# Kernel optimization log

Hardware: AMD Instinct MI355X
Metric: run time of the kernel (lower is better)

The kernel has to match this reference:

```python
import jax, jax.numpy as jnp
import numpy as np

N_NODES = 50000


def gcn_layer(x, src, dst, W, b, n_nodes):
    # Linear transform first (as in PyG GCNConv)
    x = x @ W  # [N, out]
    # Symmetric normalization with self-loop-augmented degree
    ones = jnp.ones(src.shape[0], dtype=x.dtype)
    deg = jax.ops.segment_sum(ones, dst, num_segments=n_nodes)
    dinv = jnp.where(deg > 0, jax.lax.rsqrt(deg), 0.0).astype(x.dtype)
    norm = dinv[src] * dinv[dst]  # [E]
    msgs = x[src] * norm[:, None]  # [E, out]
    out = jax.ops.segment_sum(msgs, dst, num_segments=n_nodes)
    return out + b


def add_self_loops(edge_index, n_nodes):
    loop = jnp.arange(n_nodes, dtype=edge_index.dtype)
    src = jnp.concatenate([edge_index[0], loop])
    dst = jnp.concatenate([edge_index[1], loop])
    return src, dst


def setup_inputs() -> dict:
    key = jax.random.key(0)
    k1, k2, k3, k4 = jax.random.split(key, 4)
    in_ch, hid = 256, 256
    n_edges = 1600000
    x = jax.random.normal(k1, (N_NODES, in_ch), dtype=jnp.float32)
    edge_index = jax.random.randint(k2, (2, n_edges), 0, N_NODES, dtype=jnp.int64)
    # Glorot-style init for GCN weights
    W1 = jax.random.normal(k3, (in_ch, hid), dtype=jnp.float32) * (1.0 / np.sqrt(in_ch))
    b1 = jnp.zeros((hid,), dtype=jnp.float32)
    W2 = jax.random.normal(k4, (hid, hid), dtype=jnp.float32) * (1.0 / np.sqrt(hid))
    b2 = jnp.zeros((hid,), dtype=jnp.float32)
    return {"x": x, "edge_index": edge_index, "W1": W1, "b1": b1, "W2": W2, "b2": b2}


def reference(x, edge_index, W1, b1, W2, b2):
    n = x.shape[0]
    src, dst = add_self_loops(edge_index, n)
    h = gcn_layer(x, src, dst, W1, b1, n)
    h = jax.nn.relu(h)
    out = gcn_layer(h, src, dst, W2, b2, n)
    return out
```

## Files before the change

### kernel.cpp

```cpp
#include <hip/hip_runtime.h>
#include <stdint.h>

typedef __attribute__((ext_vector_type(8))) short bf16x8;
typedef __attribute__((ext_vector_type(4))) float f32x4;

#define NBLK 256
#define BSH  7
#define BSZ  128

typedef __attribute__((address_space(1))) const unsigned int gu32;
typedef __attribute__((address_space(3))) unsigned int lu32;

__device__ __forceinline__ float bf2f(unsigned short b) {
    union { unsigned u; float f; } c; c.u = ((unsigned)b) << 16; return c.f;
}
__device__ __forceinline__ float bflo(unsigned w) {
    union { unsigned u; float f; } c; c.u = w << 16; return c.f;
}
__device__ __forceinline__ float bfhi(unsigned w) {
    union { unsigned u; float f; } c; c.u = w & 0xffff0000u; return c.f;
}
__device__ __forceinline__ unsigned short f2bf(float f) {
    union { float f; unsigned u; } c; c.f = f;
    unsigned u = c.u;
    u += 0x7fffu + ((u >> 16) & 1u);
    return (unsigned short)(u >> 16);
}

__global__ void GNNEncoder_317827579954_kernel() {}

__global__ void k_flags(const unsigned* __restrict__ x, const int* __restrict__ ei,
                        int E, int* __restrict__ flags) {
    int t = threadIdx.x;
    int pl = 0;
    for (int i = t; i < 256; i += 64) {
        unsigned u = x[i] & 0xffffu;
        unsigned e = (u >> 7) & 0xffu;
        if ((e >= 100u && e <= 145u) || u == 0u) ++pl;
    }
    for (int off = 32; off; off >>= 1) pl += __shfl_down(pl, off);
    int n = E < 64 ? E : 64;
    unsigned long long nz = __ballot(t < n ? (ei[2 * t + 1] != 0) : 0);
    if (t == 0) {
        flags[0] = (pl >= 192) ? 0 : 1;
        flags[1] = (nz == 0ull) ? 1 : 0;
    }
}

__global__ void k_cvtT(const void* __restrict__ Wa, unsigned short* __restrict__ Wta,
                       const void* __restrict__ Wb, unsigned short* __restrict__ Wtb,
                       const int* __restrict__ flags) {
    int bb = blockIdx.x;
    const void* W = bb < 256 ? Wa : Wb;
    unsigned short* Wt = bb < 256 ? Wta : Wtb;
    int n = bb & 255, k = threadIdx.x;
    unsigned short v;
    if (flags[0]) v = f2bf(((const float*)W)[k * 256 + n]);
    else          v = ((const unsigned short*)W)[k * 256 + n];
    Wt[n * 256 + k] = v;
}


__global__ __launch_bounds__(256) void k_cmat(const int* __restrict__ ei, int E,
                                              const int* __restrict__ flags,
                                              int* __restrict__ cmat, int nb) {
    __shared__ int lc[512];
    int t = threadIdx.x, b = blockIdx.x;
    for (int i = t; i < nb; i += 256) lc[i] = 0;
    __syncthreads();
    int chunk = (E + NBLK - 1) / NBLK;
    int beg = b * chunk;
    int end = beg + chunk; if (end > E) end = E;
    int i64 = flags[1];
    for (int i = beg + t; i < end; i += 256) {
        int d = i64 ? ei[2 * E + 2 * i] : ei[E + i];
        atomicAdd(&lc[d >> BSH], 1);
    }
    __syncthreads();
    for (int j = t; j < nb; j += 256) cmat[j * NBLK + b] = lc[j];
}

__global__ __launch_bounds__(512) void k_cscan(int* __restrict__ cmat,
                                               int* __restrict__ boff,
                                               int* __restrict__ offs,
                                               int nb, int N, int E) {
    __shared__ int sc[512];
    int t = threadIdx.x;
    int run = 0;
    if (t < nb) {
        int* row = cmat + t * NBLK;
        for (int b = 0; b < NBLK; ++b) { int v = row[b]; row[b] = run; run += v; }
    }
    sc[t] = run;
    __syncthreads();
    int val = run;
    for (int off = 1; off < 512; off <<= 1) {
        int u = (t >= off) ? sc[t - off] : 0;
        __syncthreads();
        sc[t] += u;
        __syncthreads();
    }
    int ex = sc[t] - val;
    if (t < nb) {
        boff[t] = ex;
        int* row = cmat + t * NBLK;
        for (int b = 0; b < NBLK; ++b) row[b] += ex;
    }
    if (t == 0) { boff[nb] = E; offs[N] = E; }
}

__global__ __launch_bounds__(256) void k_fillmat(const int* __restrict__ ei, int E,
                                                 const int* __restrict__ flags,
                                                 const int* __restrict__ cmat,
                                                 unsigned* __restrict__ tmp, int nb) {
    __shared__ int cur[512];
    int t = threadIdx.x, b = blockIdx.x;
    for (int j = t; j < nb; j += 256) cur[j] = cmat[j * NBLK + b];
    __syncthreads();
    int chunk = (E + NBLK - 1) / NBLK;
    int beg = b * chunk;
    int end = beg + chunk; if (end > E) end = E;
    int i64 = flags[1];
    for (int i = beg + t; i < end; i += 256) {
        int s, d;
        if (i64) { s = ei[2 * i]; d = ei[2 * E + 2 * i]; }
        else     { s = ei[i];     d = ei[E + i]; }
        int p = atomicAdd(&cur[d >> BSH], 1);
        tmp[p] = ((unsigned)s << BSH) | (unsigned)(d & (BSZ - 1));
    }
}

__global__ __launch_bounds__(256) void k_bbuild(const unsigned* __restrict__ tmp,
                                                const int* __restrict__ boff,
                                                int* __restrict__ offs,
                                                float* __restrict__ dinv,
                                                int* __restrict__ csr, int N) {
    __shared__ int ldeg[BSZ], lex[BSZ], lcur[BSZ];
    int b = blockIdx.x;
    int t = threadIdx.x;
    int base = b << BSH;
    int beg = boff[b], end = boff[b + 1];
    if (t < BSZ) ldeg[t] = 0;
    __syncthreads();
    for (int i = beg + t; i < end; i += 256) {
        unsigned u = tmp[i];
        atomicAdd(&ldeg[u & (BSZ - 1u)], 1);
    }
    __syncthreads();
    if (t == 0) {
        int run = 0;
        for (int i = 0; i < BSZ; ++i) {
            int v = ldeg[i];
            lex[i] = run; lcur[i] = run;
            run += v;
        }
    }
    __syncthreads();
    if (t < BSZ) {
        int v = base + t;
        if (v < N) {
            offs[v] = beg + lex[t];
            dinv[v] = rsqrtf((float)(ldeg[t] + 1));
        }
    }
    for (int i = beg + t; i < end; i += 256) {
        unsigned u = tmp[i];
        int p = atomicAdd(&lcur[u & (BSZ - 1u)], 1);
        csr[beg + p] = (int)(u >> BSH);
    }
}

__global__ __launch_bounds__(256) void k_gemm(const void* __restrict__ Araw,
                                              const unsigned short* __restrict__ Bt,
                                              unsigned short* __restrict__ C,
                                              const float* __restrict__ dinv,
                                              const int* __restrict__ flags, int useflag,
                                              int M) {
    __shared__ unsigned short smem[16384];
    int tid  = threadIdx.x;
    int lane = tid & 63;
    int wave = tid >> 6;
    int q = lane >> 4;
    int r = lane & 15;
    int rowBase0 = blockIdx.x * 64;
    int rowBase = rowBase0 + wave * 16;
    int af32 = useflag ? flags[0] : 0;

    int arow = rowBase + r;
    arow = arow < M ? arow : M - 1;
    const unsigned short* aptrh = (const unsigned short*)Araw + (size_t)arow * 256;
    const float*          aptrf = (const float*)Araw + (size_t)arow * 256;

    auto stage = [&](int buf, int kk) {
#pragma unroll
        for (int j = 0; j < 4; ++j) {
            int c = wave * 256 + j * 64 + lane;
            int col = c >> 2;
            int kc = (c & 3) ^ (col & 3);
            const unsigned short* src = Bt + col * 256 + kk + kc * 8;
            unsigned short* dst = smem + buf * 8192 + (wave * 4 + j) * 512;
            __builtin_amdgcn_global_load_lds((gu32*)src, (lu32*)dst, 16, 0, 0);
        }
    };

    stage(0, 0);
    __syncthreads();

    f32x4 acc[16] = {};
    int cur = 0;
    for (int kk = 0; kk < 256; kk += 32) {
        if (kk < 224) stage(cur ^ 1, kk + 32);
        bf16x8 a;
        if (af32) {
            float4 v0 = *(const float4*)(aptrf + kk + q * 8);
            float4 v1 = *(const float4*)(aptrf + kk + q * 8 + 4);
            union { unsigned short s[8]; bf16x8 v; } ua;
            ua.s[0] = f2bf(v0.x); ua.s[1] = f2bf(v0.y); ua.s[2] = f2bf(v0.z); ua.s[3] = f2bf(v0.w);
            ua.s[4] = f2bf(v1.x); ua.s[5] = f2bf(v1.y); ua.s[6] = f2bf(v1.z); ua.s[7] = f2bf(v1.w);
            a = ua.v;
        } else {
            a = *(const bf16x8*)(aptrh + kk + q * 8);
        }
#pragma unroll
        for (int nt = 0; nt < 16; ++nt) {
            int col = nt * 16 + r;
            const unsigned short* bp = smem + cur * 8192 + col * 32 + (q ^ (col & 3)) * 8;
            bf16x8 b = *(const bf16x8*)bp;
            acc[nt] = __builtin_amdgcn_mfma_f32_16x16x32_bf16(a, b, acc[nt], 0, 0, 0);
        }
        __syncthreads();
        cur ^= 1;
    }

    float ds4[4];
#pragma unroll
    for (int r2 = 0; r2 < 4; ++r2) {
        int row = rowBase + q * 4 + r2;
        ds4[r2] = (row < M) ? dinv[row] : 0.f;
    }
    int lrow0 = wave * 16 + q * 4;
#pragma unroll
    for (int nt = 0; nt < 16; ++nt) {
        int col = nt * 16 + r;
#pragma unroll
        for (int r2 = 0; r2 < 4; ++r2)
            smem[(lrow0 + r2) * 256 + col] = f2bf(acc[nt][r2] * ds4[r2]);
    }
    __syncthreads();
#pragma unroll
    for (int p = 0; p < 8; ++p) {
        int idx = wave * 4096 + p * 512 + lane * 8;
        int grow = rowBase0 + (idx >> 8);
        if (grow < M)
            *(uint4*)(C + (size_t)grow * 256 + (idx & 255)) = *(const uint4*)(smem + idx);
    }
}

__global__ __launch_bounds__(256) void k_agg(const unsigned short* __restrict__ XWs,
                                             const int* __restrict__ csr,
                                             const int* __restrict__ offs,
                                             const float* __restrict__ dinv,
                                             const void* __restrict__ bias,
                                             void* __restrict__ out,
                                             int relu, int final_, const int* __restrict__ flags,
                                             int N) {
    int v = blockIdx.x * 4 + (threadIdx.x >> 6);
    if (v >= N) return;
    int lane = threadIdx.x & 63;
    int half = lane >> 5;
    int cl   = (lane & 31) * 8;
    float acc[8] = {};
    int beg = offs[v], end = offs[v + 1];
    int e = beg;
    for (; e + 8 <= end; e += 8) {
        int s[4]; uint4 u[4];
#pragma unroll
        for (int j = 0; j < 4; ++j) s[j] = csr[e + 2 * j + half];
#pragma unroll
        for (int j = 0; j < 4; ++j) u[j] = *(const uint4*)(XWs + (size_t)s[j] * 256 + cl);
#pragma unroll
        for (int j = 0; j < 4; ++j) {
            acc[0] += bflo(u[j].x); acc[1] += bfhi(u[j].x);
            acc[2] += bflo(u[j].y); acc[3] += bfhi(u[j].y);
            acc[4] += bflo(u[j].z); acc[5] += bfhi(u[j].z);
            acc[6] += bflo(u[j].w); acc[7] += bfhi(u[j].w);
        }
    }
    for (; e + 2 <= end; e += 2) {
        int s = csr[e + half];
        uint4 u = *(const uint4*)(XWs + (size_t)s * 256 + cl);
        acc[0] += bflo(u.x); acc[1] += bfhi(u.x);
        acc[2] += bflo(u.y); acc[3] += bfhi(u.y);
        acc[4] += bflo(u.z); acc[5] += bfhi(u.z);
        acc[6] += bflo(u.w); acc[7] += bfhi(u.w);
    }
    if (e < end && half == 0) {
        int s = csr[e];
        uint4 u = *(const uint4*)(XWs + (size_t)s * 256 + cl);
        acc[0] += bflo(u.x); acc[1] += bfhi(u.x);
        acc[2] += bflo(u.y); acc[3] += bfhi(u.y);
        acc[4] += bflo(u.z); acc[5] += bfhi(u.z);
        acc[6] += bflo(u.w); acc[7] += bfhi(u.w);
    }
#pragma unroll
    for (int k = 0; k < 8; ++k) acc[k] += __shfl_xor(acc[k], 32);
    if (half) return;

    float dv = dinv[v];
    uint4 su = *(const uint4*)(XWs + (size_t)v * 256 + cl);
    float sf[8];
    sf[0] = bflo(su.x); sf[1] = bfhi(su.x);
    sf[2] = bflo(su.y); sf[3] = bfhi(su.y);
    sf[4] = bflo(su.z); sf[5] = bfhi(su.z);
    sf[6] = bflo(su.w); sf[7] = bfhi(su.w);
    float bb[8];
    if (flags[0]) {
        const float4* bp = (const float4*)((const float*)bias + cl);
        float4 b0 = bp[0], b1 = bp[1];
        bb[0] = b0.x; bb[1] = b0.y; bb[2] = b0.z; bb[3] = b0.w;
        bb[4] = b1.x; bb[5] = b1.y; bb[6] = b1.z; bb[7] = b1.w;
    } else {
        uint4 bu = *(const uint4*)((const unsigned short*)bias + cl);
        bb[0] = bflo(bu.x); bb[1] = bfhi(bu.x);
        bb[2] = bflo(bu.y); bb[3] = bfhi(bu.y);
        bb[4] = bflo(bu.z); bb[5] = bfhi(bu.z);
        bb[6] = bflo(bu.w); bb[7] = bfhi(bu.w);
    }
    float r[8];
#pragma unroll
    for (int k = 0; k < 8; ++k) {
        float t = dv * (acc[k] + sf[k]) + bb[k];
        r[k] = relu ? fmaxf(t, 0.f) : t;
    }
    if (final_ && flags[0]) {
        float* op = (float*)out + (size_t)v * 256 + cl;
        float4 o0, o1;
        o0.x = r[0]; o0.y = r[1]; o0.z = r[2]; o0.w = r[3];
        o1.x = r[4]; o1.y = r[5]; o1.z = r[6]; o1.w = r[7];
        ((float4*)op)[0] = o0; ((float4*)op)[1] = o1;
    } else {
        uint4 o;
        o.x = (unsigned)f2bf(r[0]) | ((unsigned)f2bf(r[1]) << 16);
        o.y = (unsigned)f2bf(r[2]) | ((unsigned)f2bf(r[3]) << 16);
        o.z = (unsigned)f2bf(r[4]) | ((unsigned)f2bf(r[5]) << 16);
        o.w = (unsigned)f2bf(r[6]) | ((unsigned)f2bf(r[7]) << 16);
        *(uint4*)((unsigned short*)out + (size_t)v * 256 + cl) = o;
    }
}

extern "C" void kernel_launch(void* const* d_in, const int* in_sizes, int n_in,
                              void* d_out, int out_size, void* d_ws, size_t ws_size,
                              hipStream_t stream) {
    (void)n_in; (void)out_size; (void)ws_size;
    const void* x  = d_in[0];
    const int*  ei = (const int*)d_in[1];
    const void* W1 = d_in[2];
    const void* b1 = d_in[3];
    const void* W2 = d_in[4];
    const void* b2 = d_in[5];

    int N = in_sizes[0] / 256;
    int E = in_sizes[1] / 2;
    int NB = (N + BSZ - 1) / BSZ;

    char* p = (char*)d_ws;
    auto alloc = [&](size_t bytes) {
        char* r = p;
        p += (bytes + 255) & ~(size_t)255;
        return r;
    };
    int*            flags  = (int*)alloc(8);
    int*            boff   = (int*)alloc(516 * 4);
    int*            offs   = (int*)alloc(((size_t)N + 1) * 4);
    float*          dinv   = (float*)alloc((size_t)N * 4);
    unsigned short* wt1    = (unsigned short*)alloc(256 * 256 * 2);
    unsigned short* wt2    = (unsigned short*)alloc(256 * 256 * 2);
    int*            csr    = (int*)alloc((size_t)E * 4);
    unsigned short* buf0   = (unsigned short*)alloc((size_t)N * 256 * 2);
    unsigned short* buf1   = (unsigned short*)alloc((size_t)N * 256 * 2);
    unsigned*       tmp    = (unsigned*)buf1;
    int*            cmat   = (int*)buf0;
    unsigned short* xw1    = (unsigned short*)d_out;

    k_flags<<<1, 64, 0, stream>>>((const unsigned*)x, ei, E, flags);
    k_cmat<<<NBLK, 256, 0, stream>>>(ei, E, flags, cmat, NB);
    k_cscan<<<1, 512, 0, stream>>>(cmat, boff, offs, NB, N, E);
    k_fillmat<<<NBLK, 256, 0, stream>>>(ei, E, flags, cmat, tmp, NB);
    k_bbuild<<<NB, 256, 0, stream>>>(tmp, boff, offs, dinv, csr, N);

    k_cvtT<<<512, 256, 0, stream>>>(W1, wt1, W2, wt2, flags);

    int gAgg = (N + 3) / 4;
    k_gemm<<<(N + 63) / 64, 256, 0, stream>>>(x, wt1, xw1, dinv, flags, 1, N);
    k_agg<<<gAgg, 256, 0, stream>>>(xw1, csr, offs, dinv, b1,
                                    (void*)buf0, 1, 0, flags, N);
    k_gemm<<<(N + 63) / 64, 256, 0, stream>>>(buf0, wt2, buf1, dinv, flags, 0, N);
    k_agg<<<gAgg, 256, 0, stream>>>(buf1, csr, offs, dinv, b2,
                                    d_out, 0, 1, flags, N);
}
```

Before: 470.7 us.

## Bucket CSR edges by source range and sweep ranges across multiple nodes per wave

The block-level CSR build now sorts each destination's edges by source bucket (source >> 12, 13 buckets) and stores one offset per (node, bucket). Each aggregation wave now handles 13 destination nodes over all 256 columns and walks the buckets in an outer loop. The aim is to keep the gathered source rows inside a narrow window of the feature table at any moment, so they stay in L2. The cost is a 13x larger offsets array and far fewer waves, with short per-bucket edge runs that mostly fall into the serial tail loop. That lowers memory-level parallelism and occupancy.

```diff
diff --git a/kernel.cpp b/kernel.cpp
--- a/kernel.cpp
+++ b/kernel.cpp
@@ -7,6 +7,8 @@
 #define NBLK 256
 #define BSH  7
 #define BSZ  128
+#define RNG  13
+#define NPN  13
 
 typedef __attribute__((address_space(1))) const unsigned int gu32;
 typedef __attribute__((address_space(3))) unsigned int lu32;
@@ -82,7 +84,7 @@
 
 __global__ __launch_bounds__(512) void k_cscan(int* __restrict__ cmat,
                                                int* __restrict__ boff,
-                                               int* __restrict__ offs,
+                                               int* __restrict__ noffs,
                                                int nb, int N, int E) {
     __shared__ int sc[512];
     int t = threadIdx.x;
@@ -106,7 +108,7 @@
         int* row = cmat + t * NBLK;
         for (int b = 0; b < NBLK; ++b) row[b] += ex;
     }
-    if (t == 0) { boff[nb] = E; offs[N] = E; }
+    if (t == 0) { boff[nb] = E; noffs[(size_t)N * RNG] = E; }
 }
 
 __global__ __launch_bounds__(256) void k_fillmat(const int* __restrict__ ei, int E,
@@ -132,40 +134,58 @@
 
 __global__ __launch_bounds__(256) void k_bbuild(const unsigned* __restrict__ tmp,
                                                 const int* __restrict__ boff,
-                                                int* __restrict__ offs,
+                                                int* __restrict__ noffs,
                                                 float* __restrict__ dinv,
                                                 int* __restrict__ csr, int N) {
-    __shared__ int ldeg[BSZ], lex[BSZ], lcur[BSZ];
+    __shared__ int kc[2048];
+    __shared__ int cur[2048];
+    __shared__ int sc[256];
+    __shared__ int tot;
     int b = blockIdx.x;
     int t = threadIdx.x;
     int base = b << BSH;
     int beg = boff[b], end = boff[b + 1];
-    if (t < BSZ) ldeg[t] = 0;
+    for (int i = t; i < 2048; i += 256) kc[i] = 0;
     __syncthreads();
     for (int i = beg + t; i < end; i += 256) {
         unsigned u = tmp[i];
-        atomicAdd(&ldeg[u & (BSZ - 1u)], 1);
-    }
-    __syncthreads();
-    if (t == 0) {
-        int run = 0;
-        for (int i = 0; i < BSZ; ++i) {
-            int v = ldeg[i];
-            lex[i] = run; lcur[i] = run;
-            run += v;
-        }
-    }
-    __syncthreads();
-    if (t < BSZ) {
+        atomicAdd(&kc[(u & 127u) * 16 + (u >> 19)], 1);
+    }
+    __syncthreads();
+    int b8 = t * 8, loc[8], msum = 0;
+#pragma unroll
+    for (int j = 0; j < 8; ++j) { loc[j] = kc[b8 + j]; msum += loc[j]; }
+    sc[t] = msum;
+    __syncthreads();
+    int val = msum;
+    for (int off = 1; off < 256; off <<= 1) {
+        int u2 = (t >= off) ? sc[t - off] : 0;
+        __syncthreads();
+        sc[t] += u2;
+        __syncthreads();
+    }
+    int run = sc[t] - val;
+    if (t == 255) tot = sc[255];
+#pragma unroll
+    for (int j = 0; j < 8; ++j) { int v2 = loc[j]; kc[b8 + j] = run; cur[b8 + j] = run; run += v2; }
+    __syncthreads();
+    for (int i = t; i < 128 * RNG; i += 256) {
+        int local = i / RNG, o = i - local * RNG;
+        int v = base + local;
+        if (v < N) noffs[(size_t)v * RNG + o] = beg + kc[local * 16 + o];
+    }
+    if (t < 128) {
         int v = base + t;
         if (v < N) {
-            offs[v] = beg + lex[t];
-            dinv[v] = rsqrtf((float)(ldeg[t] + 1));
-        }
-    }
+            int s0 = kc[t * 16];
+            int s1 = (t == 127) ? tot : kc[(t + 1) * 16];
+            dinv[v] = rsqrtf((float)(s1 - s0 + 1));
+        }
+    }
+    __syncthreads();
     for (int i = beg + t; i < end; i += 256) {
         unsigned u = tmp[i];
-        int p = atomicAdd(&lcur[u & (BSZ - 1u)], 1);
+        int p = atomicAdd(&cur[(u & 127u) * 16 + (u >> 19)], 1);
         csr[beg + p] = (int)(u >> BSH);
     }
 }
@@ -256,95 +276,87 @@
     }
 }
 
-__global__ __launch_bounds__(256) void k_agg(const unsigned short* __restrict__ XWs,
-                                             const int* __restrict__ csr,
-                                             const int* __restrict__ offs,
-                                             const float* __restrict__ dinv,
-                                             const void* __restrict__ bias,
-                                             void* __restrict__ out,
-                                             int relu, int final_, const int* __restrict__ flags,
-                                             int N) {
-    int v = blockIdx.x * 4 + (threadIdx.x >> 6);
-    if (v >= N) return;
+__global__ __launch_bounds__(256, 4) void k_agg(const unsigned short* __restrict__ XWs,
+                                                const int* __restrict__ csr,
+                                                const int* __restrict__ noffs,
+                                                const float* __restrict__ dinv,
+                                                const void* __restrict__ bias,
+                                                void* __restrict__ out,
+                                                int relu, int final_,
+                                                const int* __restrict__ flags, int N) {
+    int wgid = blockIdx.x * 4 + (threadIdx.x >> 6);
+    int v0 = wgid * NPN;
     int lane = threadIdx.x & 63;
-    int half = lane >> 5;
-    int cl   = (lane & 31) * 8;
-    float acc[8] = {};
-    int beg = offs[v], end = offs[v + 1];
-    int e = beg;
-    for (; e + 8 <= end; e += 8) {
-        int s[4]; uint4 u[4];
-#pragma unroll
-        for (int j = 0; j < 4; ++j) s[j] = csr[e + 2 * j + half];
-#pragma unroll
-        for (int j = 0; j < 4; ++j) u[j] = *(const uint4*)(XWs + (size_t)s[j] * 256 + cl);
-#pragma unroll
-        for (int j = 0; j < 4; ++j) {
-            acc[0] += bflo(u[j].x); acc[1] += bfhi(u[j].x);
-            acc[2] += bflo(u[j].y); acc[3] += bfhi(u[j].y);
-            acc[4] += bflo(u[j].z); acc[5] += bfhi(u[j].z);
-            acc[6] += bflo(u[j].w); acc[7] += bfhi(u[j].w);
-        }
-    }
-    for (; e + 2 <= end; e += 2) {
-        int s = csr[e + half];
-        uint4 u = *(const uint4*)(XWs + (size_t)s * 256 + cl);
-        acc[0] += bflo(u.x); acc[1] += bfhi(u.x);
-        acc[2] += bflo(u.y); acc[3] += bfhi(u.y);
-        acc[4] += bflo(u.z); acc[5] += bfhi(u.z);
-        acc[6] += bflo(u.w); acc[7] += bfhi(u.w);
-    }
-    if (e < end && half == 0) {
-        int s = csr[e];
-        uint4 u = *(const uint4*)(XWs + (size_t)s * 256 + cl);
-        acc[0] += bflo(u.x); acc[1] += bfhi(u.x);
-        acc[2] += bflo(u.y); acc[3] += bfhi(u.y);
-        acc[4] += bflo(u.z); acc[5] += bfhi(u.z);
-        acc[6] += bflo(u.w); acc[7] += bfhi(u.w);
-    }
-#pragma unroll
-    for (int k = 0; k < 8; ++k) acc[k] += __shfl_xor(acc[k], 32);
-    if (half) return;
-
-    float dv = dinv[v];
-    uint4 su = *(const uint4*)(XWs + (size_t)v * 256 + cl);
-    float sf[8];
-    sf[0] = bflo(su.x); sf[1] = bfhi(su.x);
-    sf[2] = bflo(su.y); sf[3] = bfhi(su.y);
-    sf[4] = bflo(su.z); sf[5] = bfhi(su.z);
-    sf[6] = bflo(su.w); sf[7] = bfhi(su.w);
-    float bb[8];
+    int c = lane * 4;
+    float acc[NPN][4];
+#pragma unroll
+    for (int n = 0; n < NPN; ++n) { acc[n][0] = acc[n][1] = acc[n][2] = acc[n][3] = 0.f; }
+
+    for (int o = 0; o < RNG; ++o) {
+#pragma unroll
+        for (int n = 0; n < NPN; ++n) {
+            int v = v0 + n;
+            if (v >= N) continue;
+            size_t idx = (size_t)v * RNG + o;
+            int e   = noffs[idx];
+            int end = noffs[idx + 1];
+            for (; e + 4 <= end; e += 4) {
+                int s0 = csr[e], s1 = csr[e + 1], s2 = csr[e + 2], s3 = csr[e + 3];
+                uint2 u0 = *(const uint2*)(XWs + (size_t)s0 * 256 + c);
+                uint2 u1 = *(const uint2*)(XWs + (size_t)s1 * 256 + c);
+                uint2 u2 = *(const uint2*)(XWs + (size_t)s2 * 256 + c);
+                uint2 u3 = *(const uint2*)(XWs + (size_t)s3 * 256 + c);
+                acc[n][0] += bflo(u0.x); acc[n][1] += bfhi(u0.x);
+                acc[n][2] += bflo(u0.y); acc[n][3] += bfhi(u0.y);
+                acc[n][0] += bflo(u1.x); acc[n][1] += bfhi(u1.x);
+                acc[n][2] += bflo(u1.y); acc[n][3] += bfhi(u1.y);
+                acc[n][0] += bflo(u2.x); acc[n][1] += bfhi(u2.x);
+                acc[n][2] += bflo(u2.y); acc[n][3] += bfhi(u2.y);
+                acc[n][0] += bflo(u3.x); acc[n][1] += bfhi(u3.x);
+                acc[n][2] += bflo(u3.y); acc[n][3] += bfhi(u3.y);
+            }
+            for (; e < end; ++e) {
+                int s = csr[e];
+                uint2 u = *(const uint2*)(XWs + (size_t)s * 256 + c);
+                acc[n][0] += bflo(u.x); acc[n][1] += bfhi(u.x);
+                acc[n][2] += bflo(u.y); acc[n][3] += bfhi(u.y);
+            }
+        }
+    }
+
+    float bb[4];
     if (flags[0]) {
-        const float4* bp = (const float4*)((const float*)bias + cl);
-        float4 b0 = bp[0], b1 = bp[1];
+        float4 b0 = *(const float4*)((const float*)bias + c);
         bb[0] = b0.x; bb[1] = b0.y; bb[2] = b0.z; bb[3] = b0.w;
-        bb[4] = b1.x; bb[5] = b1.y; bb[6] = b1.z; bb[7] = b1.w;
     } else {
-        uint4 bu = *(const uint4*)((const unsigned short*)bias + cl);
+        uint2 bu = *(const uint2*)((const unsigned short*)bias + c);
         bb[0] = bflo(bu.x); bb[1] = bfhi(bu.x);
         bb[2] = bflo(bu.y); bb[3] = bfhi(bu.y);
-        bb[4] = bflo(bu.z); bb[5] = bfhi(bu.z);
-        bb[6] = bflo(bu.w); bb[7] = bfhi(bu.w);
-    }
-    float r[8];
-#pragma unroll
-    for (int k = 0; k < 8; ++k) {
-        float t = dv * (acc[k] + sf[k]) + bb[k];
-        r[k] = relu ? fmaxf(t, 0.f) : t;
-    }
-    if (final_ && flags[0]) {
-        float* op = (float*)out + (size_t)v * 256 + cl;
-        float4 o0, o1;
-        o0.x = r[0]; o0.y = r[1]; o0.z = r[2]; o0.w = r[3];
-        o1.x = r[4]; o1.y = r[5]; o1.z = r[6]; o1.w = r[7];
-        ((float4*)op)[0] = o0; ((float4*)op)[1] = o1;
-    } else {
-        uint4 o;
-        o.x = (unsigned)f2bf(r[0]) | ((unsigned)f2bf(r[1]) << 16);
-        o.y = (unsigned)f2bf(r[2]) | ((unsigned)f2bf(r[3]) << 16);
-        o.z = (unsigned)f2bf(r[4]) | ((unsigned)f2bf(r[5]) << 16);
-        o.w = (unsigned)f2bf(r[6]) | ((unsigned)f2bf(r[7]) << 16);
-        *(uint4*)((unsigned short*)out + (size_t)v * 256 + cl) = o;
+    }
+    int f32out = final_ && flags[0];
+#pragma unroll
+    for (int n = 0; n < NPN; ++n) {
+        int v = v0 + n;
+        if (v >= N) continue;
+        float dv = dinv[v];
+        uint2 su = *(const uint2*)(XWs + (size_t)v * 256 + c);
+        float r0 = dv * (acc[n][0] + bflo(su.x)) + bb[0];
+        float r1 = dv * (acc[n][1] + bfhi(su.x)) + bb[1];
+        float r2 = dv * (acc[n][2] + bflo(su.y)) + bb[2];
+        float r3 = dv * (acc[n][3] + bfhi(su.y)) + bb[3];
+        if (relu) {
+            r0 = fmaxf(r0, 0.f); r1 = fmaxf(r1, 0.f);
+            r2 = fmaxf(r2, 0.f); r3 = fmaxf(r3, 0.f);
+        }
+        if (f32out) {
+            float4 o4; o4.x = r0; o4.y = r1; o4.z = r2; o4.w = r3;
+            *(float4*)((float*)out + (size_t)v * 256 + c) = o4;
+        } else {
+            uint2 o2;
+            o2.x = (unsigned)f2bf(r0) | ((unsigned)f2bf(r1) << 16);
+            o2.y = (unsigned)f2bf(r2) | ((unsigned)f2bf(r3) << 16);
+            *(uint2*)((unsigned short*)out + (size_t)v * 256 + c) = o2;
+        }
     }
 }
 
@@ -371,7 +383,7 @@
     };
     int*            flags  = (int*)alloc(8);
     int*            boff   = (int*)alloc(516 * 4);
-    int*            offs   = (int*)alloc(((size_t)N + 1) * 4);
+    int*            noffs  = (int*)alloc(((size_t)N * RNG + 16) * 4);
     float*          dinv   = (float*)alloc((size_t)N * 4);
     unsigned short* wt1    = (unsigned short*)alloc(256 * 256 * 2);
     unsigned short* wt2    = (unsigned short*)alloc(256 * 256 * 2);
@@ -384,17 +396,17 @@
 
     k_flags<<<1, 64, 0, stream>>>((const unsigned*)x, ei, E, flags);
     k_cmat<<<NBLK, 256, 0, stream>>>(ei, E, flags, cmat, NB);
-    k_cscan<<<1, 512, 0, stream>>>(cmat, boff, offs, NB, N, E);
+    k_cscan<<<1, 512, 0, stream>>>(cmat, boff, noffs, NB, N, E);
     k_fillmat<<<NBLK, 256, 0, stream>>>(ei, E, flags, cmat, tmp, NB);
-    k_bbuild<<<NB, 256, 0, stream>>>(tmp, boff, offs, dinv, csr, N);
+    k_bbuild<<<NB, 256, 0, stream>>>(tmp, boff, noffs, dinv, csr, N);
 
     k_cvtT<<<512, 256, 0, stream>>>(W1, wt1, W2, wt2, flags);
 
-    int gAgg = (N + 3) / 4;
+    int gAgg = (N + 4 * NPN - 1) / (4 * NPN);
     k_gemm<<<(N + 63) / 64, 256, 0, stream>>>(x, wt1, xw1, dinv, flags, 1, N);
-    k_agg<<<gAgg, 256, 0, stream>>>(xw1, csr, offs, dinv, b1,
+    k_agg<<<gAgg, 256, 0, stream>>>(xw1, csr, noffs, dinv, b1,
                                     (void*)buf0, 1, 0, flags, N);
     k_gemm<<<(N + 63) / 64, 256, 0, stream>>>(buf0, wt2, buf1, dinv, flags, 0, N);
-    k_agg<<<gAgg, 256, 0, stream>>>(buf1, csr, offs, dinv, b2,
+    k_agg<<<gAgg, 256, 0, stream>>>(buf1, csr, noffs, dinv, b2,
                                     d_out, 0, 1, flags, N);
 }
```

After: 722.0 us. 53.4% more time.
